# Optimization experiments

Measured on AMD Instinct MI355X. Metric: run time of the kernel, lower is better.

The kernel has to match this reference:

```python
import jax, jax.numpy as jnp
import numpy as np

N_NODES = 10000
N_REL = 200
DIM = 128          # rank * 2
REL_DIM = 128
VIS_DIM = 512
TXT_DIM = 768
N_EDGES = 320000


def _glorot(key, shape):
    fan_in, fan_out = shape[1], shape[0]
    lim = (6.0 / (fan_in + fan_out)) ** 0.5
    return jax.random.uniform(key, shape, jnp.float32, -lim, lim)


def setup_inputs() -> dict:
    key = jax.random.key(0)
    ks = jax.random.split(key, 24)
    inp = {}
    inp['x'] = jax.random.randint(ks[0], (1024, 3), 0, N_NODES)
    inp['edge_index'] = jax.random.randint(ks[1], (2, N_EDGES), 0, N_NODES)
    inp['edge_type'] = jax.random.randint(ks[2], (N_EDGES,), 0, N_REL)
    inp['visual'] = jax.random.normal(ks[3], (N_NODES, VIS_DIM), jnp.float32)
    inp['textual'] = jax.random.normal(ks[4], (N_NODES, TXT_DIM), jnp.float32)
    # embeddings (scaled by 0.001 as in torch init)
    inp['structural_emb'] = jax.random.normal(ks[5], (N_NODES, DIM), jnp.float32) * 0.001
    inp['relation_emb'] = jax.random.normal(ks[6], (N_REL, REL_DIM), jnp.float32) * 0.001
    # three KBGAT convs: w1 [out, 2*in+rel], b1 [out], w2 [1, out]
    cat = 2 * DIM + REL_DIM
    for i, tag in enumerate(['s', 'v', 't']):
        inp[f'W1_{tag}'] = _glorot(ks[7 + 3 * i], (DIM, cat))
        inp[f'b1_{tag}'] = jnp.zeros((DIM,), jnp.float32)
        inp[f'w2_{tag}'] = _glorot(ks[8 + 3 * i], (1, DIM))
    # modality projections
    inp['Wv'] = _glorot(ks[16], (DIM, VIS_DIM))
    inp['bv'] = jnp.zeros((DIM,), jnp.float32)
    inp['Wt'] = _glorot(ks[17], (DIM, TXT_DIM))
    inp['bt'] = jnp.zeros((DIM,), jnp.float32)
    inp['alpha'] = jnp.float32(0.1)
    inp['gamma'] = jnp.float32(0.8)
    return inp


def kbgat_conv(feat, rel_emb, src, dst, edge_type, W1, b1, w2):
    # gather per-edge embeddings: x_i = target, x_j = source (PyG default flow)
    triple = jnp.concatenate([feat[dst], feat[src], rel_emb[edge_type]], axis=1)  # [E, 2*D+R]
    c = triple @ W1.T + b1                                   # [E, D]
    b = jax.nn.leaky_relu(c @ w2[0])                         # [E]
    # segment softmax over destination nodes
    m = jax.ops.segment_max(b, dst, num_segments=N_NODES)
    e = jnp.exp(b - m[dst])
    z = jax.ops.segment_sum(e, dst, num_segments=N_NODES)
    attn = e / z[dst]                                        # [E]
    agg = jax.ops.segment_sum(c * attn[:, None], dst, num_segments=N_NODES)  # [N, D]
    return jax.nn.leaky_relu(agg)


def reference(x, edge_index, edge_type, visual, textual, structural_emb, relation_emb,
              W1_s, b1_s, w2_s, W1_v, b1_v, w2_v, W1_t, b1_t, w2_t,
              Wv, bv, Wt, bt, alpha, gamma):
    src, dst = edge_index[0], edge_index[1]
    h_s = kbgat_conv(structural_emb, relation_emb, src, dst, edge_type, W1_s, b1_s, w2_s)
    vf = visual @ Wv.T + bv
    h_v = kbgat_conv(vf, relation_emb, src, dst, edge_type, W1_v, b1_v, w2_v)
    tf = textual @ Wt.T + bt
    h_t = kbgat_conv(tf, relation_emb, src, dst, edge_type, W1_t, b1_t, w2_t)
    return (1.0 - alpha - gamma) * h_s + alpha * h_v + gamma * h_t
```

## Files before the change

### kernel.cpp

```cpp
#include <hip/hip_runtime.h>
#include <hip/hip_bf16.h>

typedef unsigned short u16;
typedef unsigned int u32;
typedef __bf16 bf16x8 __attribute__((ext_vector_type(8)));
typedef float f32x4 __attribute__((ext_vector_type(4)));

#define DIM 128
#define NTMAX 24

__device__ __forceinline__ u16 f2bf_rne(float x) {
  u32 u = __float_as_uint(x);
  return (u16)((u + 0x7fffu + ((u >> 16) & 1u)) >> 16);
}
__device__ __forceinline__ float lrelu(float x) { return x > 0.f ? x : 0.01f * x; }
__device__ __forceinline__ int iclamp(int v, int hi) { return v < 0 ? 0 : (v >= hi ? hi - 1 : v); }
__device__ __forceinline__ float sane(float x) { return (x == x) ? x : 0.f; }

__device__ __forceinline__ float wred_max(float v) {
  #pragma unroll
  for (int o = 32; o > 0; o >>= 1) v = fmaxf(v, __shfl_xor(v, o, 64));
  return v;
}
__device__ __forceinline__ float wred_sum(float v) {
  #pragma unroll
  for (int o = 32; o > 0; o >>= 1) v += __shfl_xor(v, o, 64);
  return v;
}

__global__ void hist_k(const int* __restrict__ dst, int* __restrict__ cnt, int E, int N) {
  int e = blockIdx.x * blockDim.x + threadIdx.x;
  if (e < E) {
    int d = dst[e];
    if (d >= 0 && d < N) atomicAdd(&cnt[d], 1);
  }
}

__global__ __launch_bounds__(1024) void scan_k(const int* __restrict__ cnt,
                                               int* __restrict__ offs, int N) {
  __shared__ int sums[1024];
  int t = threadIdx.x;
  int chunk = (N + 1023) >> 10;
  int base = t * chunk;
  int s = 0;
  for (int i = 0; i < chunk; ++i) { int idx = base + i; if (idx < N) s += cnt[idx]; }
  sums[t] = s;
  __syncthreads();
  for (int off = 1; off < 1024; off <<= 1) {
    int v = (t >= off) ? sums[t - off] : 0;
    __syncthreads();
    sums[t] += v;
    __syncthreads();
  }
  int prefix = (t > 0) ? sums[t - 1] : 0;
  for (int i = 0; i < chunk; ++i) {
    int idx = base + i;
    if (idx < N) { offs[idx] = prefix; prefix += cnt[idx]; }
  }
  if (t == 1023) offs[N] = sums[1023];
}

__global__ void scatter_k(const int* __restrict__ dst, const int* __restrict__ src,
                          const int* __restrict__ etyp,
                          const int* __restrict__ offs,
                          int* __restrict__ cursor, u32* __restrict__ sortedST,
                          int E, int N, int NR) {
  int e = blockIdx.x * blockDim.x + threadIdx.x;
  if (e < E) {
    int d = dst[e];
    if (d >= 0 && d < N) {
      int pos = offs[d] + atomicAdd(&cursor[d], 1);
      if (pos >= 0 && pos < E) {
        u32 s = (u32)iclamp(src[e], N);
        u32 t = (u32)iclamp(etyp[e], NR);
        sortedST[pos] = (t << 16) | s;
      }
    }
  }
}

struct PrepArgs {
  const float* W1[3]; const float* Wmod[3]; int K[3]; int isCopy[3];
  u16* Wc[3];
};
struct PrArgs {
  const float* rel; const float* W1[3]; const float* b1[3];
  const float* bmod[3]; const float* w2[3];
  u16* PrAll; float* qr[3]; int NR;
};
struct GArgs {
  const float* A[3]; const u16* B[3]; const float* w2[3];
  u16* PdAll; u16* PsAll; float* qd[3]; float* qs[3];
  int M; int K[3];
};
struct AgArgs {
  const u32* sortedST; const int* offs;
  const float* qd[3]; const float* qs[3]; const float* qr[3];
  const u16* PdAll; const u16* PsAll; const u16* PrAll;
  const float* alphaP; const float* gammaP;
  float* outp; int N; int NR; int E;
};

__global__ void prep_wc_all(PrepArgs a) {
  int m = blockIdx.z;
  int K = a.K[m];
  int k = blockIdx.x * blockDim.x + threadIdx.x;
  int o = blockIdx.y;
  if (k >= K) return;
  int half = (o >= 128) ? 128 : 0;
  int oo = o & 127;
  const float* W1 = a.W1[m];
  float acc;
  if (a.isCopy[m]) {
    acc = W1[oo * 384 + half + k];
  } else {
    const float* Wm = a.Wmod[m];
    acc = 0.f;
    for (int i = 0; i < 128; ++i)
      acc += W1[oo * 384 + half + i] * Wm[i * K + k];
  }
  a.Wc[m][((size_t)(k >> 5) * 256 + o) * 32 + (k & 31)] = f2bf_rne(acc);
}

__global__ __launch_bounds__(128) void prep_pr_all(PrArgs a) {
  __shared__ float red[128];
  int m = blockIdx.z;
  int r = blockIdx.x;
  if (r >= a.NR) return;
  int o = threadIdx.x;
  const float* W1 = a.W1[m];
  float acc = a.b1[m][o];
  for (int i = 0; i < 128; ++i)
    acc += W1[o * 384 + 256 + i] * a.rel[r * 128 + i];
  const float* bmod = a.bmod[m];
  if (bmod != nullptr) {
    for (int i = 0; i < 128; ++i)
      acc += (W1[o * 384 + i] + W1[o * 384 + 128 + i]) * bmod[i];
  }
  a.PrAll[(size_t)r * 384 + m * 128 + o] = f2bf_rne(acc);
  red[o] = acc * a.w2[m][o];
  __syncthreads();
  for (int s = 64; s > 0; s >>= 1) {
    if (o < s) red[o] += red[o + s];
    __syncthreads();
  }
  if (o == 0) a.qr[m][r] = sane(red[0]);
}

__global__ __launch_bounds__(256) void gemm_fused(GArgs g) {
  __shared__ u16 Als[NTMAX * 16 * 32];
  __shared__ float qpart[4][16];
  int m = blockIdx.y;
  int M = g.M, K = g.K[m];
  int nt = K >> 5;
  const u16* Bpk = g.B[m];
  const float* w2 = g.w2[m];
  int tid = threadIdx.x;
  int lane = tid & 63, wv = tid >> 6;
  int quad = lane >> 4, l16 = lane & 15;
  int row0 = blockIdx.x * 16;

  {
    int srow = tid >> 4;
    int scol = (tid & 15) * 2;
    int gr = row0 + srow;
    bool v = gr < M;
    const float* Ag = g.A[m] + (size_t)(v ? gr : 0) * K;
    for (int kb = 0; kb < nt; ++kb) {
      float2 x = make_float2(0.f, 0.f);
      if (v) x = *reinterpret_cast<const float2*>(Ag + kb * 32 + scol);
      *reinterpret_cast<u32*>(&Als[(kb * 16 + srow) * 32 + scol]) =
          (u32)f2bf_rne(x.x) | ((u32)f2bf_rne(x.y) << 16);
    }
  }
  __syncthreads();

  const u16* Bpg = Bpk + (size_t)(wv * 64 + l16) * 32 + quad * 8;

  f32x4 acc[4];
  #pragma unroll
  for (int t = 0; t < 4; ++t) acc[t] = (f32x4){0.f, 0.f, 0.f, 0.f};

  bf16x8 bc[8];
  {
    const u16* p0 = Bpg;
    const u16* p1 = Bpg + ((1 < nt) ? 8192 : 0);
    bc[0] = *reinterpret_cast<const bf16x8*>(p0);
    bc[1] = *reinterpret_cast<const bf16x8*>(p0 + 512);
    bc[2] = *reinterpret_cast<const bf16x8*>(p0 + 1024);
    bc[3] = *reinterpret_cast<const bf16x8*>(p0 + 1536);
    bc[4] = *reinterpret_cast<const bf16x8*>(p1);
    bc[5] = *reinterpret_cast<const bf16x8*>(p1 + 512);
    bc[6] = *reinterpret_cast<const bf16x8*>(p1 + 1024);
    bc[7] = *reinterpret_cast<const bf16x8*>(p1 + 1536);
  }

  for (int kb = 0; kb < nt; kb += 2) {
    int kn0 = (kb + 2 < nt) ? kb + 2 : kb;
    int kn1 = (kb + 3 < nt) ? kb + 3 : kb;
    const u16* pn0 = Bpg + (size_t)kn0 * 8192;
    const u16* pn1 = Bpg + (size_t)kn1 * 8192;
    bf16x8 bn[8];
    bn[0] = *reinterpret_cast<const bf16x8*>(pn0);
    bn[1] = *reinterpret_cast<const bf16x8*>(pn0 + 512);
    bn[2] = *reinterpret_cast<const bf16x8*>(pn0 + 1024);
    bn[3] = *reinterpret_cast<const bf16x8*>(pn0 + 1536);
    bn[4] = *reinterpret_cast<const bf16x8*>(pn1);
    bn[5] = *reinterpret_cast<const bf16x8*>(pn1 + 512);
    bn[6] = *reinterpret_cast<const bf16x8*>(pn1 + 1024);
    bn[7] = *reinterpret_cast<const bf16x8*>(pn1 + 1536);

    bf16x8 a0 = *reinterpret_cast<const bf16x8*>(&Als[(kb * 16 + l16) * 32 + quad * 8]);
    bf16x8 a1 = *reinterpret_cast<const bf16x8*>(&Als[((kb + 1) * 16 + l16) * 32 + quad * 8]);

    acc[0] = __builtin_amdgcn_mfma_f32_16x16x32_bf16(a0, bc[0], acc[0], 0, 0, 0);
    acc[1] = __builtin_amdgcn_mfma_f32_16x16x32_bf16(a0, bc[1], acc[1], 0, 0, 0);
    acc[2] = __builtin_amdgcn_mfma_f32_16x16x32_bf16(a0, bc[2], acc[2], 0, 0, 0);
    acc[3] = __builtin_amdgcn_mfma_f32_16x16x32_bf16(a0, bc[3], acc[3], 0, 0, 0);
    acc[0] = __builtin_amdgcn_mfma_f32_16x16x32_bf16(a1, bc[4], acc[0], 0, 0, 0);
    acc[1] = __builtin_amdgcn_mfma_f32_16x16x32_bf16(a1, bc[5], acc[1], 0, 0, 0);
    acc[2] = __builtin_amdgcn_mfma_f32_16x16x32_bf16(a1, bc[6], acc[2], 0, 0, 0);
    acc[3] = __builtin_amdgcn_mfma_f32_16x16x32_bf16(a1, bc[7], acc[3], 0, 0, 0);

    #pragma unroll
    for (int u = 0; u < 8; ++u) bc[u] = bn[u];
  }

  u16* PdAll = g.PdAll;
  u16* PsAll = g.PsAll;
  float w2c[4];
  #pragma unroll
  for (int t = 0; t < 4; ++t) w2c[t] = w2[(wv & 1) * 64 + t * 16 + l16];

  float part[4];
  #pragma unroll
  for (int r = 0; r < 4; ++r) {
    int rr = row0 + quad * 4 + r;
    bool ok = rr < M;
    float qp = 0.f;
    #pragma unroll
    for (int t = 0; t < 4; ++t) {
      int c = (wv & 1) * 64 + t * 16 + l16;
      if (ok) {
        if (wv < 2) PdAll[(size_t)rr * 384 + m * 128 + c] = f2bf_rne(acc[t][r]);
        else        PsAll[(size_t)rr * 384 + m * 128 + c] = f2bf_rne(acc[t][r]);
      }
      qp += acc[t][r] * w2c[t];
    }
    #pragma unroll
    for (int mk = 1; mk < 16; mk <<= 1) qp += __shfl_xor(qp, mk, 64);
    part[r] = qp;
  }
  if (l16 == 0) {
    #pragma unroll
    for (int r = 0; r < 4; ++r) qpart[wv][quad * 4 + r] = part[r];
  }
  __syncthreads();
  if (tid < 32) {
    int row = tid & 15;
    int rr = row0 + row;
    if (rr < M) {
      if (tid < 16) g.qd[m][rr] = sane(qpart[0][row] + qpart[1][row]);
      else          g.qs[m][rr] = sane(qpart[2][row] + qpart[3][row]);
    }
  }
}

__global__ __launch_bounds__(256) void aggregate_all(AgArgs a) {
  int n = blockIdx.x * 4 + (threadIdx.x >> 6);
  if (n >= a.N) return;
  int lane = threadIdx.x & 63;
  int E = a.E;
  int eb = a.offs[n], ee = a.offs[n + 1];
  if (eb < 0) eb = 0;
  if (eb > E) eb = E;
  if (ee < eb) ee = eb;
  if (ee > E) ee = E;
  int En = ee - eb;

  float al = a.alphaP[0];
  if (!(al > 0.f && al < 1.f)) al = 0.1f;
  float ga = a.gammaP[0];
  if (!(ga > 0.f && ga < 1.f)) ga = 0.8f;
  float coef[3] = {1.f - al - ga, al, ga};

  float qdn[3];
  #pragma unroll
  for (int m = 0; m < 3; ++m) qdn[m] = sane(a.qd[m][n]);

  const u16* PsAll = a.PsAll;
  const u16* PrAll = a.PrAll;
  int dlo = 2 * lane;

  float rm[3] = {-1e30f, -1e30f, -1e30f};
  float z[3] = {0.f, 0.f, 0.f};
  float a0[3] = {0.f, 0.f, 0.f};
  float a1[3] = {0.f, 0.f, 0.f};
  for (int c0 = 0; c0 < En; c0 += 64) {
    int cn = min(64, En - c0);
    u32 stp = 0;
    float bm[3] = {-1e30f, -1e30f, -1e30f};
    if (lane < cn) {
      stp = a.sortedST[eb + c0 + lane];
      int s = (int)(stp & 0xffffu);
      int t = (int)(stp >> 16);
      #pragma unroll
      for (int m = 0; m < 3; ++m)
        bm[m] = lrelu(qdn[m] + a.qs[m][s] + a.qr[m][t]);
    }
    float wr[3];
    #pragma unroll
    for (int m = 0; m < 3; ++m) {
      float cm = wred_max(bm[m]);
      float nm = fmaxf(rm[m], cm);
      float sc = __expf(fmaxf(rm[m] - nm, -80.f));
      z[m] *= sc; a0[m] *= sc; a1[m] *= sc;
      rm[m] = nm;
      wr[m] = (lane < cn) ? __expf(fmaxf(bm[m] - nm, -80.f)) : 0.f;
      z[m] += wr[m];
    }

    int cnR = (cn + 3) & ~3;
    for (int j = 0; j < cnR; j += 4) {
      u32 stj[4];
      float wj[4][3];
      #pragma unroll
      for (int u = 0; u < 4; ++u) {
        stj[u] = __shfl(stp, j + u, 64);
        wj[u][0] = __shfl(wr[0], j + u, 64);
        wj[u][1] = __shfl(wr[1], j + u, 64);
        wj[u][2] = __shfl(wr[2], j + u, 64);
      }
      u32 pu[4][3], ru[4][3];
      #pragma unroll
      for (int u = 0; u < 4; ++u) {
        const u16* ps = PsAll + (size_t)(stj[u] & 0xffffu) * 384 + dlo;
        const u16* pr = PrAll + (size_t)(stj[u] >> 16) * 384 + dlo;
        #pragma unroll
        for (int m = 0; m < 3; ++m) {
          pu[u][m] = *reinterpret_cast<const u32*>(ps + m * 128);
          ru[u][m] = *reinterpret_cast<const u32*>(pr + m * 128);
        }
      }
      #pragma unroll
      for (int u = 0; u < 4; ++u) {
        #pragma unroll
        for (int m = 0; m < 3; ++m) {
          float ps0 = __uint_as_float(pu[u][m] << 16);
          float ps1 = __uint_as_float(pu[u][m] & 0xffff0000u);
          float pr0 = __uint_as_float(ru[u][m] << 16);
          float pr1 = __uint_as_float(ru[u][m] & 0xffff0000u);
          a0[m] = fmaf(wj[u][m], ps0 + pr0, a0[m]);
          a1[m] = fmaf(wj[u][m], ps1 + pr1, a1[m]);
        }
      }
    }
  }
  #pragma unroll
  for (int m = 0; m < 3; ++m) z[m] = wred_sum(z[m]);

  float o0 = 0.f, o1 = 0.f;
  const u16* pd = a.PdAll + (size_t)n * 384 + dlo;
  #pragma unroll
  for (int m = 0; m < 3; ++m) {
    float h0 = 0.f, h1 = 0.f;
    if (En > 0 && z[m] > 0.f) {
      float rz = 1.f / z[m];
      u32 du = *reinterpret_cast<const u32*>(pd + m * 128);
      float pd0 = __uint_as_float(du << 16), pd1 = __uint_as_float(du & 0xffff0000u);
      h0 = lrelu(pd0 + a0[m] * rz);
      h1 = lrelu(pd1 + a1[m] * rz);
    }
    o0 = fmaf(coef[m], h0, o0);
    o1 = fmaf(coef[m], h1, o1);
  }
  float* op = a.outp + (size_t)n * 128 + dlo;
  op[0] = sane(o0);
  op[1] = sane(o1);
}

extern "C" void kernel_launch(void* const* d_in, const int* in_sizes, int n_in,
                              void* d_out, int out_size, void* d_ws, size_t ws_size,
                              hipStream_t stream) {
  const int* ei        = (const int*)d_in[1];
  const int* et        = (const int*)d_in[2];
  const float* visual  = (const float*)d_in[3];
  const float* textual = (const float*)d_in[4];
  const float* semb    = (const float*)d_in[5];
  const float* relemb  = (const float*)d_in[6];
  const float* W1s = (const float*)d_in[7];
  const float* b1s = (const float*)d_in[8];
  const float* w2s = (const float*)d_in[9];
  const float* W1v = (const float*)d_in[10];
  const float* b1v = (const float*)d_in[11];
  const float* w2v = (const float*)d_in[12];
  const float* W1t = (const float*)d_in[13];
  const float* b1t = (const float*)d_in[14];
  const float* w2t = (const float*)d_in[15];
  const float* Wv  = (const float*)d_in[16];
  const float* bv  = (const float*)d_in[17];
  const float* Wt  = (const float*)d_in[18];
  const float* bt  = (const float*)d_in[19];
  const float* alphaP = (const float*)d_in[20];
  const float* gammaP = (const float*)d_in[21];
  float* outp = (float*)d_out;

  const int E   = in_sizes[2];
  const int N   = in_sizes[5] / DIM;
  const int NR  = in_sizes[6] / DIM;
  const int VIS = in_sizes[3] / N;
  const int TXT = in_sizes[4] / N;
  const int KMAX = (TXT > VIS) ? TXT : VIS;
  int Ks[3] = {DIM, VIS, TXT};
  const int NT16 = (N + 15) / 16;

  const float* W1a[3]   = {W1s, W1v, W1t};
  const float* b1a[3]   = {b1s, b1v, b1t};
  const float* w2a[3]   = {w2s, w2v, w2t};
  const float* Wmoda[3] = {nullptr, Wv, Wt};
  const float* bmoda[3] = {nullptr, bv, bt};
  const float* Amoda[3] = {semb, visual, textual};

  const int* esrc = ei;
  const int* edst = ei + E;
  int egrid = (E + 255) / 256;

  size_t off = 0;
  auto take = [&](size_t bytes) -> size_t {
    size_t o = off;
    off = (off + bytes + 255) & ~(size_t)255;
    return o;
  };
  size_t o_cnt  = take((size_t)2 * N * 4);
  size_t o_offs = take((size_t)(N + 1) * 4);
  size_t o_st   = take((size_t)E * 4);
  size_t meta_end = off;
  size_t o_qdm[3], o_qsm[3], o_qrm[3], o_Wcm[3];
  for (int m = 0; m < 3; ++m) {
    o_qdm[m] = take((size_t)N * 4);
    o_qsm[m] = take((size_t)N * 4);
    o_qrm[m] = take((size_t)NR * 4);
    o_Wcm[m] = take((size_t)256 * Ks[m] * 2);
  }
  size_t o_PrAll = take((size_t)NR * 384 * 2);
  size_t o_PdAll = take((size_t)N * 384 * 2);
  size_t o_PsAll = take((size_t)N * 384 * 2);
  size_t need = off;

  if (ws_size < need) {
    hipMemsetAsync(d_out, 0, (size_t)out_size * 4, stream);
    return;
  }

  char* w = (char*)d_ws;
  int* counts = (int*)(w + o_cnt);
  int* cursor = counts + N;
  int* offs   = (int*)(w + o_offs);
  u32* sortedST = (u32*)(w + o_st);

  hipMemsetAsync(w, 0, meta_end, stream);
  hist_k<<<egrid, 256, 0, stream>>>(edst, counts, E, N);
  scan_k<<<1, 1024, 0, stream>>>(counts, offs, N);
  scatter_k<<<egrid, 256, 0, stream>>>(edst, esrc, et, offs, cursor, sortedST, E, N, NR);

  PrepArgs pa;
  PrArgs ra;
  GArgs ga;
  AgArgs aa;
  ra.rel = relemb; ra.NR = NR;
  ra.PrAll = (u16*)(w + o_PrAll);
  ga.M = N;
  ga.PdAll = (u16*)(w + o_PdAll);
  ga.PsAll = (u16*)(w + o_PsAll);
  for (int m = 0; m < 3; ++m) {
    pa.W1[m] = W1a[m]; pa.Wmod[m] = Wmoda[m]; pa.K[m] = Ks[m];
    pa.isCopy[m] = (m == 0);
    pa.Wc[m] = (u16*)(w + o_Wcm[m]);
    ra.W1[m] = W1a[m]; ra.b1[m] = b1a[m]; ra.bmod[m] = bmoda[m]; ra.w2[m] = w2a[m];
    ra.qr[m] = (float*)(w + o_qrm[m]);
    ga.A[m] = Amoda[m]; ga.B[m] = (const u16*)(w + o_Wcm[m]); ga.w2[m] = w2a[m];
    ga.qd[m] = (float*)(w + o_qdm[m]); ga.qs[m] = (float*)(w + o_qsm[m]);
    ga.K[m] = Ks[m];
    aa.qd[m] = (const float*)(w + o_qdm[m]);
    aa.qs[m] = (const float*)(w + o_qsm[m]);
    aa.qr[m] = (const float*)(w + o_qrm[m]);
  }
  aa.PdAll = (const u16*)(w + o_PdAll);
  aa.PsAll = (const u16*)(w + o_PsAll);
  aa.PrAll = (const u16*)(w + o_PrAll);
  aa.sortedST = sortedST; aa.offs = offs;
  aa.alphaP = alphaP; aa.gammaP = gammaP;
  aa.outp = outp; aa.N = N; aa.NR = NR; aa.E = E;

  prep_wc_all<<<dim3((KMAX + 255) / 256, 256, 3), 256, 0, stream>>>(pa);
  prep_pr_all<<<dim3(NR, 1, 3), 128, 0, stream>>>(ra);
  gemm_fused<<<dim3(NT16, 3), 256, 0, stream>>>(ga);
  aggregate_all<<<(N + 3) / 4, 256, 0, stream>>>(aa);
}
```

Before: 290.0 us.

## Tile node GEMM over 64 rows with K-chunked shared staging

The fused node-feature GEMM now gives each block 64 rows instead of 16. Each B fragment loaded from global memory is reused across four 16-row groups, which cuts weight traffic per row by four. The A tile is staged through shared memory in 256-wide K chunks with float4 loads, and the old register double-buffered prefetch of B is dropped. The grid shrinks to about 157 blocks per modality, which may underfill the GPU, and loads are no longer software-pipelined.

```diff
diff --git a/kernel.cpp b/kernel.cpp
--- a/kernel.cpp
+++ b/kernel.cpp
@@ -7,11 +7,13 @@
 typedef float f32x4 __attribute__((ext_vector_type(4)));
 
 #define DIM 128
-#define NTMAX 24
 
 __device__ __forceinline__ u16 f2bf_rne(float x) {
   u32 u = __float_as_uint(x);
   return (u16)((u + 0x7fffu + ((u >> 16) & 1u)) >> 16);
+}
+__device__ __forceinline__ u32 packbf2(float x, float y) {
+  return (u32)f2bf_rne(x) | ((u32)f2bf_rne(y) << 16);
 }
 __device__ __forceinline__ float lrelu(float x) { return x > 0.f ? x : 0.01f * x; }
 __device__ __forceinline__ int iclamp(int v, int hi) { return v < 0 ? 0 : (v >= hi ? hi - 1 : v); }
@@ -148,8 +150,8 @@
 }
 
 __global__ __launch_bounds__(256) void gemm_fused(GArgs g) {
-  __shared__ u16 Als[NTMAX * 16 * 32];
-  __shared__ float qpart[4][16];
+  __shared__ u16 Als[8 * 64 * 32];
+  __shared__ float qpart[4][64];
   int m = blockIdx.y;
   int M = g.M, K = g.K[m];
   int nt = K >> 5;
@@ -158,72 +160,56 @@
   int tid = threadIdx.x;
   int lane = tid & 63, wv = tid >> 6;
   int quad = lane >> 4, l16 = lane & 15;
-  int row0 = blockIdx.x * 16;
-
-  {
-    int srow = tid >> 4;
-    int scol = (tid & 15) * 2;
-    int gr = row0 + srow;
-    bool v = gr < M;
-    const float* Ag = g.A[m] + (size_t)(v ? gr : 0) * K;
-    for (int kb = 0; kb < nt; ++kb) {
-      float2 x = make_float2(0.f, 0.f);
-      if (v) x = *reinterpret_cast<const float2*>(Ag + kb * 32 + scol);
-      *reinterpret_cast<u32*>(&Als[(kb * 16 + srow) * 32 + scol]) =
-          (u32)f2bf_rne(x.x) | ((u32)f2bf_rne(x.y) << 16);
-    }
-  }
-  __syncthreads();
+  int row0 = blockIdx.x * 64;
+
+  int srow = tid >> 2;
+  int kseg = (tid & 3) * 64;
+  int grow = row0 + srow;
+  if (grow >= M) grow = M - 1;
+  const float* Ag = g.A[m] + (size_t)grow * K;
 
   const u16* Bpg = Bpk + (size_t)(wv * 64 + l16) * 32 + quad * 8;
 
-  f32x4 acc[4];
-  #pragma unroll
-  for (int t = 0; t < 4; ++t) acc[t] = (f32x4){0.f, 0.f, 0.f, 0.f};
-
-  bf16x8 bc[8];
-  {
-    const u16* p0 = Bpg;
-    const u16* p1 = Bpg + ((1 < nt) ? 8192 : 0);
-    bc[0] = *reinterpret_cast<const bf16x8*>(p0);
-    bc[1] = *reinterpret_cast<const bf16x8*>(p0 + 512);
-    bc[2] = *reinterpret_cast<const bf16x8*>(p0 + 1024);
-    bc[3] = *reinterpret_cast<const bf16x8*>(p0 + 1536);
-    bc[4] = *reinterpret_cast<const bf16x8*>(p1);
-    bc[5] = *reinterpret_cast<const bf16x8*>(p1 + 512);
-    bc[6] = *reinterpret_cast<const bf16x8*>(p1 + 1024);
-    bc[7] = *reinterpret_cast<const bf16x8*>(p1 + 1536);
-  }
-
-  for (int kb = 0; kb < nt; kb += 2) {
-    int kn0 = (kb + 2 < nt) ? kb + 2 : kb;
-    int kn1 = (kb + 3 < nt) ? kb + 3 : kb;
-    const u16* pn0 = Bpg + (size_t)kn0 * 8192;
-    const u16* pn1 = Bpg + (size_t)kn1 * 8192;
-    bf16x8 bn[8];
-    bn[0] = *reinterpret_cast<const bf16x8*>(pn0);
-    bn[1] = *reinterpret_cast<const bf16x8*>(pn0 + 512);
-    bn[2] = *reinterpret_cast<const bf16x8*>(pn0 + 1024);
-    bn[3] = *reinterpret_cast<const bf16x8*>(pn0 + 1536);
-    bn[4] = *reinterpret_cast<const bf16x8*>(pn1);
-    bn[5] = *reinterpret_cast<const bf16x8*>(pn1 + 512);
-    bn[6] = *reinterpret_cast<const bf16x8*>(pn1 + 1024);
-    bn[7] = *reinterpret_cast<const bf16x8*>(pn1 + 1536);
-
-    bf16x8 a0 = *reinterpret_cast<const bf16x8*>(&Als[(kb * 16 + l16) * 32 + quad * 8]);
-    bf16x8 a1 = *reinterpret_cast<const bf16x8*>(&Als[((kb + 1) * 16 + l16) * 32 + quad * 8]);
-
-    acc[0] = __builtin_amdgcn_mfma_f32_16x16x32_bf16(a0, bc[0], acc[0], 0, 0, 0);
-    acc[1] = __builtin_amdgcn_mfma_f32_16x16x32_bf16(a0, bc[1], acc[1], 0, 0, 0);
-    acc[2] = __builtin_amdgcn_mfma_f32_16x16x32_bf16(a0, bc[2], acc[2], 0, 0, 0);
-    acc[3] = __builtin_amdgcn_mfma_f32_16x16x32_bf16(a0, bc[3], acc[3], 0, 0, 0);
-    acc[0] = __builtin_amdgcn_mfma_f32_16x16x32_bf16(a1, bc[4], acc[0], 0, 0, 0);
-    acc[1] = __builtin_amdgcn_mfma_f32_16x16x32_bf16(a1, bc[5], acc[1], 0, 0, 0);
-    acc[2] = __builtin_amdgcn_mfma_f32_16x16x32_bf16(a1, bc[6], acc[2], 0, 0, 0);
-    acc[3] = __builtin_amdgcn_mfma_f32_16x16x32_bf16(a1, bc[7], acc[3], 0, 0, 0);
-
+  f32x4 acc[4][4];
+  #pragma unroll
+  for (int rg = 0; rg < 4; ++rg)
     #pragma unroll
-    for (int u = 0; u < 8; ++u) bc[u] = bn[u];
+    for (int t = 0; t < 4; ++t) acc[rg][t] = (f32x4){0.f, 0.f, 0.f, 0.f};
+
+  int nchunk = (nt + 7) >> 3;
+  for (int c = 0; c < nchunk; ++c) {
+    int kbase = c << 8;
+    __syncthreads();
+    #pragma unroll
+    for (int i = 0; i < 16; ++i) {
+      int kl = kseg + i * 4;
+      int kg = kbase + kl;
+      if (kg < K) {
+        float4 v = *reinterpret_cast<const float4*>(Ag + kg);
+        u32* d = reinterpret_cast<u32*>(&Als[((kl >> 5) * 64 + srow) * 32 + (kl & 31)]);
+        d[0] = packbf2(v.x, v.y);
+        d[1] = packbf2(v.z, v.w);
+      }
+    }
+    __syncthreads();
+    int kbR = nt - (c << 3);
+    if (kbR > 8) kbR = 8;
+    for (int kbl = 0; kbl < kbR; ++kbl) {
+      const u16* bp = Bpg + (size_t)((c << 3) + kbl) * 8192;
+      bf16x8 b0 = *reinterpret_cast<const bf16x8*>(bp);
+      bf16x8 b1 = *reinterpret_cast<const bf16x8*>(bp + 512);
+      bf16x8 b2 = *reinterpret_cast<const bf16x8*>(bp + 1024);
+      bf16x8 b3 = *reinterpret_cast<const bf16x8*>(bp + 1536);
+      #pragma unroll
+      for (int rg = 0; rg < 4; ++rg) {
+        bf16x8 a = *reinterpret_cast<const bf16x8*>(
+            &Als[(kbl * 64 + rg * 16 + l16) * 32 + quad * 8]);
+        acc[rg][0] = __builtin_amdgcn_mfma_f32_16x16x32_bf16(a, b0, acc[rg][0], 0, 0, 0);
+        acc[rg][1] = __builtin_amdgcn_mfma_f32_16x16x32_bf16(a, b1, acc[rg][1], 0, 0, 0);
+        acc[rg][2] = __builtin_amdgcn_mfma_f32_16x16x32_bf16(a, b2, acc[rg][2], 0, 0, 0);
+        acc[rg][3] = __builtin_amdgcn_mfma_f32_16x16x32_bf16(a, b3, acc[rg][3], 0, 0, 0);
+      }
+    }
   }
 
   u16* PdAll = g.PdAll;
@@ -232,36 +218,40 @@
   #pragma unroll
   for (int t = 0; t < 4; ++t) w2c[t] = w2[(wv & 1) * 64 + t * 16 + l16];
 
-  float part[4];
-  #pragma unroll
-  for (int r = 0; r < 4; ++r) {
-    int rr = row0 + quad * 4 + r;
-    bool ok = rr < M;
-    float qp = 0.f;
+  #pragma unroll
+  for (int rg = 0; rg < 4; ++rg) {
+    float part[4];
     #pragma unroll
-    for (int t = 0; t < 4; ++t) {
-      int c = (wv & 1) * 64 + t * 16 + l16;
-      if (ok) {
-        if (wv < 2) PdAll[(size_t)rr * 384 + m * 128 + c] = f2bf_rne(acc[t][r]);
-        else        PsAll[(size_t)rr * 384 + m * 128 + c] = f2bf_rne(acc[t][r]);
-      }
-      qp += acc[t][r] * w2c[t];
-    }
-    #pragma unroll
-    for (int mk = 1; mk < 16; mk <<= 1) qp += __shfl_xor(qp, mk, 64);
-    part[r] = qp;
-  }
-  if (l16 == 0) {
-    #pragma unroll
-    for (int r = 0; r < 4; ++r) qpart[wv][quad * 4 + r] = part[r];
+    for (int r = 0; r < 4; ++r) {
+      int rr = row0 + rg * 16 + quad * 4 + r;
+      bool ok = rr < M;
+      float qp = 0.f;
+      #pragma unroll
+      for (int t = 0; t < 4; ++t) {
+        int cc = (wv & 1) * 64 + t * 16 + l16;
+        if (ok) {
+          if (wv < 2) PdAll[(size_t)rr * 384 + m * 128 + cc] = f2bf_rne(acc[rg][t][r]);
+          else        PsAll[(size_t)rr * 384 + m * 128 + cc] = f2bf_rne(acc[rg][t][r]);
+        }
+        qp += acc[rg][t][r] * w2c[t];
+      }
+      #pragma unroll
+      for (int mk = 1; mk < 16; mk <<= 1) qp += __shfl_xor(qp, mk, 64);
+      part[r] = qp;
+    }
+    if (l16 == 0) {
+      #pragma unroll
+      for (int r = 0; r < 4; ++r) qpart[wv][rg * 16 + quad * 4 + r] = part[r];
+    }
   }
   __syncthreads();
-  if (tid < 32) {
-    int row = tid & 15;
+  if (tid < 128) {
+    int row = tid & 63;
+    int half = tid >> 6;
     int rr = row0 + row;
     if (rr < M) {
-      if (tid < 16) g.qd[m][rr] = sane(qpart[0][row] + qpart[1][row]);
-      else          g.qs[m][rr] = sane(qpart[2][row] + qpart[3][row]);
+      if (half == 0) g.qd[m][rr] = sane(qpart[0][row] + qpart[1][row]);
+      else           g.qs[m][rr] = sane(qpart[2][row] + qpart[3][row]);
     }
   }
 }
@@ -412,7 +402,7 @@
   const int TXT = in_sizes[4] / N;
   const int KMAX = (TXT > VIS) ? TXT : VIS;
   int Ks[3] = {DIM, VIS, TXT};
-  const int NT16 = (N + 15) / 16;
+  const int NT64 = (N + 63) / 64;
 
   const float* W1a[3]   = {W1s, W1v, W1t};
   const float* b1a[3]   = {b1s, b1v, b1t};
@@ -494,6 +484,6 @@
 
   prep_wc_all<<<dim3((KMAX + 255) / 256, 256, 3), 256, 0, stream>>>(pa);
   prep_pr_all<<<dim3(NR, 1, 3), 128, 0, stream>>>(ra);
-  gemm_fused<<<dim3(NT16, 3), 256, 0, stream>>>(ga);
+  gemm_fused<<<dim3(NT64, 3), 256, 0, stream>>>(ga);
   aggregate_all<<<(N + 3) / 4, 256, 0, stream>>>(aa);
 }
```

Result: faster. 277.2 us (-4.4%).
